# Performance work log

Measured on AMD Instinct MI355X. Metric: run time of the kernel, lower is better.

The kernel has to match this reference:

```python
import jax, jax.numpy as jnp
import numpy as np

EPS = 1e-6
B, N, I, H, O, L = 8, 2048, 64, 128, 8, 3
K = O * L
ITERS, TAU, LAM, KNN = 3, 0.1, 0.5, 5

def _ln(x, g, b):
    m = x.mean(-1, keepdims=True)
    v = jnp.mean((x - m) ** 2, -1, keepdims=True)
    return (x - m) / jnp.sqrt(v + 1e-5) * g + b

def _gelu(x):
    return jax.nn.gelu(x, approximate=False)


def setup_inputs():
    ks = jax.random.split(jax.random.key(0), 16)
    rn = lambda k, sh, s=0.05: jax.random.normal(k, sh, jnp.float32) * s
    return {
        'x': jax.random.normal(ks[0], (B, N, I), jnp.float32),
        'enc_w1': rn(ks[1], (H, I)), 'enc_b1': jnp.zeros((H,), jnp.float32),
        'enc_g1': jnp.ones((H,), jnp.float32), 'enc_bb1': jnp.zeros((H,), jnp.float32),
        'enc_w2': rn(ks[2], (H, H)), 'enc_b2': jnp.zeros((H,), jnp.float32),
        'enc_g2': jnp.ones((H,), jnp.float32), 'enc_bb2': jnp.zeros((H,), jnp.float32),
        'sp_w1': rn(ks[3], (H, H + 1)), 'sp_b1': jnp.zeros((H,), jnp.float32),
        'sp_g': jnp.ones((H,), jnp.float32), 'sp_bb': jnp.zeros((H,), jnp.float32),
        'sp_w2': rn(ks[4], (1, H), 0.005), 'sp_b2': jnp.zeros((1,), jnp.float32),
        'object_space': rn(ks[5], (1, O, H), 0.1),
        'horizon_scale': jnp.float32(0.3),
        'level_times': jnp.array([1.0, 2.5, 4.0], jnp.float32),
        'base_horizons': jnp.array([0.9, 0.6, 0.3], jnp.float32),
        'gru_w_ih': rn(ks[6], (3 * H, H)), 'gru_w_hh': rn(ks[7], (3 * H, H)),
        'gru_b_ih': jnp.zeros((3 * H,), jnp.float32), 'gru_b_hh': jnp.zeros((3 * H,), jnp.float32),
        'mlp_w1': rn(ks[8], (H, H)), 'mlp_b1': jnp.zeros((H,), jnp.float32),
        'mlp_w2': rn(ks[9], (H, H)), 'mlp_b2': jnp.zeros((H,), jnp.float32),
        'norm_g': jnp.ones((H,), jnp.float32), 'norm_b': jnp.zeros((H,), jnp.float32),
    }


def reference(x, enc_w1, enc_b1, enc_g1, enc_bb1, enc_w2, enc_b2, enc_g2, enc_bb2, sp_w1, sp_b1, sp_g, sp_bb, sp_w2, sp_b2, object_space, horizon_scale, level_times, base_horizons, gru_w_ih, gru_w_hh, gru_b_ih, gru_b_hh, mlp_w1, mlp_b1, mlp_w2, mlp_b2, norm_g, norm_b):
    # feature encoder: Linear -> LN -> GELU -> Linear -> LN
    h = _gelu(_ln(x @ enc_w1.T + enc_b1, enc_g1, enc_bb1))
    spatial = _ln(h @ enc_w2.T + enc_b2, enc_g2, enc_bb2)  # (B,N,H)
    # local density via kNN mean distance (torch.cdist equivalent)
    sq = jnp.sum(x * x, -1)
    d2 = sq[:, :, None] + sq[:, None, :] - 2.0 * jnp.einsum('bnd,bmd->bnm', x, x)
    dist = jnp.sqrt(jnp.maximum(d2, 0.0))
    knn = -jax.lax.top_k(-dist, KNN + 1)[0]           # k+1 smallest, ascending
    density = jnp.tanh(knn[..., 1:].mean(-1))          # (B,N)
    # scale predictor: Linear -> LN -> GELU -> Linear -> Softplus
    s = jnp.concatenate([spatial, density[..., None]], -1)
    s = _gelu(_ln(s @ sp_w1.T + sp_b1, sp_g, sp_bb))
    pred_scale = jax.nn.softplus(s @ sp_w2.T + sp_b2)  # (B,N,1)
    pred_time = 5.0 - 1.5 * density[..., None] + 0.5 * pred_scale
    features = jnp.concatenate([pred_time, spatial], -1)  # (B,N,H+1)
    # scale-adaptive horizons, tiled object-major to match slot layout
    hz = jnp.clip(base_horizons[None, :, None] + (horizon_scale * (density - 0.5))[:, None, :], 0.1, 1.0)
    horizons = jnp.tile(hz, (1, O, 1))                 # (B,K,N)
    # worldlines
    obj = jnp.broadcast_to(object_space, (B, O, H))
    times = jnp.broadcast_to(jnp.tile(level_times, O)[None, :, None], (B, K, 1))
    slots = jnp.concatenate([times, jnp.repeat(obj, L, axis=1)], -1)  # (B,K,H+1)
    feats_sp = features[..., 1:]
    old_flat = obj.reshape(-1, H)
    attn = None
    for _ in range(ITERS):
        diff = features[:, None, :, :] - slots[:, :, None, :]  # (B,K,N,H+1)
        dt = diff[..., 0]
        dr2 = jnp.sum(diff[..., 1:] ** 2, -1)
        ls = dt * dt - dr2
        d_L = jnp.sign(ls) * jnp.sqrt(jnp.abs(ls) + EPS)
        r = jnp.sqrt(dr2)
        cone = horizons - r / (jnp.abs(dt) + EPS) - 10.0 * jax.nn.relu(-dt) - 5.0 * jax.nn.relu(r - jnp.abs(dt))
        logits = -jnp.abs(d_L) + LAM * jnp.tanh(cone)
        attn = jax.nn.softmax(logits / TAU, axis=1)      # softmax over slots
        w = attn / (attn.sum(2, keepdims=True) + 1e-8)
        upd = jnp.einsum('bkn,bnh->bkh', w, feats_sp)
        obj_upd = upd.reshape(B, O, L, H).sum(2).reshape(-1, H)
        # GRUCell (torch semantics)
        gi = obj_upd @ gru_w_ih.T + gru_b_ih
        gh = old_flat @ gru_w_hh.T + gru_b_hh
        gi_r, gi_z, gi_n = jnp.split(gi, 3, -1)
        gh_r, gh_z, gh_n = jnp.split(gh, 3, -1)
        rg = jax.nn.sigmoid(gi_r + gh_r)
        zg = jax.nn.sigmoid(gi_z + gh_z)
        ng = jnp.tanh(gi_n + rg * gh_n)
        new = ((1.0 - zg) * ng + zg * old_flat).reshape(B, O, H)
        t = _gelu(_ln(new, norm_g, norm_b) @ mlp_w1.T + mlp_b1) @ mlp_w2.T + mlp_b2
        new = new + 0.2 * t
        slots = jnp.concatenate([times, jnp.repeat(new, L, axis=1)], -1)
    return slots, attn, pred_time[..., 0], density
```

## Files before the change

### kernel.cpp

```cpp
#include <hip/hip_runtime.h>
#include <math.h>

constexpr int cB = 8, cN = 2048, cI = 64, cH = 128, cO = 8, cK = 24;
constexpr int ROWS = cB * cN;

constexpr size_t WS_SPATIAL = 0;
constexpr size_t WS_SQ      = WS_SPATIAL + (size_t)ROWS * cH;
constexpr size_t WS_GHS     = WS_SQ + ROWS;
constexpr size_t WS_NSQ0    = WS_GHS + (size_t)cO * 3 * cH;
constexpr size_t WS_NEWOBJ  = WS_NSQ0 + cO;
constexpr size_t WS_NSQ     = WS_NEWOBJ + (size_t)cB * cO * cH;
constexpr size_t WS_WFRAG   = WS_NSQ + (size_t)cB * cO;
constexpr size_t WS_UPD3    = WS_WFRAG + 45056;
constexpr size_t WS_S3      = WS_UPD3 + (size_t)3 * cB * cK * cH;
constexpr size_t WS_XBF     = WS_S3 + (size_t)3 * cB * cK;

constexpr size_t WF_W1H = 0;
constexpr size_t WF_W1L = 8192;
constexpr size_t WF_W2H = 16384;
constexpr size_t WF_W2L = 32768;
constexpr size_t WF_WHH = 49152;
constexpr size_t WF_WHL = 69632;

constexpr size_t OUT_SLOTS = 0;
constexpr size_t OUT_ATTN  = (size_t)cB * cK * 129;
constexpr size_t OUT_PT    = OUT_ATTN + (size_t)cB * cK * cN;
constexpr size_t OUT_DEN   = OUT_PT + (size_t)cB * cN;

typedef __attribute__((ext_vector_type(8))) short bf16x8;
typedef __attribute__((ext_vector_type(4))) float f32x4;

__device__ __forceinline__ float gelu_f(float v){
  return 0.5f * v * (1.f + erff(v * 0.70710678118654752440f));
}
__device__ __forceinline__ short f2bf(float f){
  unsigned u = __float_as_uint(f);
  u += 0x7fffu + ((u >> 16) & 1u);
  return (short)(u >> 16);
}
__device__ __forceinline__ float bf2f(short h){
  return __uint_as_float(((unsigned)(unsigned short)h) << 16);
}
__device__ __forceinline__ bf16x8 pack8(float4 a, float4 b){
  bf16x8 r;
  r[0]=f2bf(a.x); r[1]=f2bf(a.y); r[2]=f2bf(a.z); r[3]=f2bf(a.w);
  r[4]=f2bf(b.x); r[5]=f2bf(b.y); r[6]=f2bf(b.z); r[7]=f2bf(b.w);
  return r;
}
__device__ __forceinline__ float qred16(float a){
  a += __shfl_xor(a, 1); a += __shfl_xor(a, 2); a += __shfl_xor(a, 4); a += __shfl_xor(a, 8);
  return a;
}
#define INS6(T0,T1,T2,T3,T4,T5,X) { \
  float _o0=T0,_o1=T1,_o2=T2,_o3=T3,_o4=T4,_o5=T5; \
  T0 = fminf(_o0, X); \
  T1 = __builtin_amdgcn_fmed3f(_o0,_o1,X); \
  T2 = __builtin_amdgcn_fmed3f(_o1,_o2,X); \
  T3 = __builtin_amdgcn_fmed3f(_o2,_o3,X); \
  T4 = __builtin_amdgcn_fmed3f(_o3,_o4,X); \
  T5 = __builtin_amdgcn_fmed3f(_o4,_o5,X); \
}
__device__ __forceinline__ void load_split_frag(const float* buf, int off, bf16x8& hi, bf16x8& lo){
  float4 u0 = *(const float4*)&buf[off];
  float4 u1 = *(const float4*)&buf[off + 4];
  float v[8] = {u0.x,u0.y,u0.z,u0.w,u1.x,u1.y,u1.z,u1.w};
  #pragma unroll
  for (int i = 0; i < 8; ++i){
    short h = f2bf(v[i]);
    hi[i] = h;
    lo[i] = f2bf(v[i] - bf2f(h));
  }
}
__device__ __forceinline__ int lidx(int row, int col, int stride){
  return row * stride + (col ^ ((row & 3) << 3));
}

__global__ __launch_bounds__(256) void k_cvt_sq(const float* __restrict__ x, short* __restrict__ xbf,
                                                float* __restrict__ sq){
  int t = threadIdx.x;
  size_t base = (size_t)blockIdx.x * 2048;
  int r = t >> 3, e0 = (t & 7) * 8;
  const float4* xp = (const float4*)(x + base + (size_t)r * cI + e0);
  float4 v0 = xp[0], v1 = xp[1];
  *(bf16x8*)(xbf + base + (size_t)r * cI + e0) = pack8(v0, v1);
  float s = v0.x*v0.x + v0.y*v0.y + v0.z*v0.z + v0.w*v0.w
          + v1.x*v1.x + v1.y*v1.y + v1.z*v1.z + v1.w*v1.w;
  s += __shfl_xor(s, 1); s += __shfl_xor(s, 2); s += __shfl_xor(s, 4);
  if ((t & 7) == 0) sq[blockIdx.x * 32 + r] = s;
}

__global__ __launch_bounds__(256) void k_prep(const float* __restrict__ objsp, const float* __restrict__ w_hh,
                                              const float* __restrict__ b_hh,
                                              const float* __restrict__ ew1, const float* __restrict__ ew2,
                                              const float* __restrict__ spw1,
                                              float* __restrict__ ghs, float* __restrict__ nsq0,
                                              short* __restrict__ wf){
  int id = blockIdx.x * 256 + threadIdx.x;
  if (id < cO * 3 * cH){
    int o = id / (3 * cH), j = id % (3 * cH);
    const float* wr = w_hh + (size_t)j * cH;
    const float* ob = objsp + (size_t)o * cH;
    float a0=0,a1=0,a2=0,a3=0;
    #pragma unroll
    for (int h = 0; h < cH; h += 4){
      a0 += wr[h]*ob[h]; a1 += wr[h+1]*ob[h+1]; a2 += wr[h+2]*ob[h+2]; a3 += wr[h+3]*ob[h+3];
    }
    ghs[id] = (a0+a1)+(a2+a3) + b_hh[j];
  } else if (id < cO * 3 * cH + cO){
    int o = id - cO * 3 * cH;
    const float* ob = objsp + (size_t)o * cH;
    float s = 0.f;
    for (int h = 0; h < cH; ++h) s += ob[h]*ob[h];
    nsq0[o] = s;
  } else {
    int idx = id - (cO * 3 * cH + cO);
    if (idx >= 45056) return;
    float w; size_t hoff, loff;
    int e, nc;
    if (idx < 8192){
      e = idx; nc = 2;
      int i = e & 7, l = (e >> 3) & 63, r = e >> 9;
      int c = r % nc, ft = r / nc;
      int f = ft * 16 + (l & 15), k = c * 32 + (l >> 4) * 8 + i;
      w = ew1[f * cI + k];
      hoff = WF_W1H + e; loff = WF_W1L + e;
    } else if (idx < 24576){
      e = idx - 8192; nc = 4;
      int i = e & 7, l = (e >> 3) & 63, r = e >> 9;
      int c = r % nc, ft = r / nc;
      int f = ft * 16 + (l & 15), k = c * 32 + (l >> 4) * 8 + i;
      w = ew2[f * cH + k];
      hoff = WF_W2H + e; loff = WF_W2L + e;
    } else {
      e = idx - 24576; nc = 5;
      int i = e & 7, l = (e >> 3) & 63, r = e >> 9;
      int c = r % nc, ft = r / nc;
      int f = ft * 16 + (l & 15), k = c * 32 + (l >> 4) * 8 + i;
      w = (k < 129) ? spw1[f * 129 + k] : 0.f;
      hoff = WF_WHH + e; loff = WF_WHL + e;
    }
    short h = f2bf(w);
    wf[hoff] = h;
    wf[loff] = f2bf(w - bf2f(h));
  }
}

__global__ __launch_bounds__(256) void k_pairwise(const short* __restrict__ xbf, const float* __restrict__ sq,
                                                  float* __restrict__ den_out){
  __shared__ float cand[4][16][101];
  int b  = blockIdx.x >> 7;
  int rt = blockIdx.x & 127;
  int r0 = rt * 16;
  int lane = threadIdx.x & 63, w = threadIdx.x >> 6;
  const short* xb = xbf + (size_t)b * cN * cI;

  int arow = r0 + (lane & 15);
  int koff = (lane >> 4) * 8;
  const bf16x8* ap = (const bf16x8*)(xb + (size_t)arow * cI + koff);
  bf16x8 a0 = ap[0];
  bf16x8 a1 = ap[4];

  float sqr[4];
  int rg0 = r0 + ((lane >> 4) << 2);
  #pragma unroll
  for (int j = 0; j < 4; ++j) sqr[j] = sq[b * cN + rg0 + j];

  float t6[4][6];
  #pragma unroll
  for (int j = 0; j < 4; ++j){
    #pragma unroll
    for (int q = 0; q < 6; ++q) t6[j][q] = 3e38f;
  }

  int cbase = w * 512;
  #pragma unroll 2
  for (int ct = 0; ct < 32; ++ct){
    int col0 = cbase + ct * 16;
    int brow = col0 + (lane & 15);
    const bf16x8* bp = (const bf16x8*)(xb + (size_t)brow * cI + koff);
    bf16x8 b0 = bp[0];
    bf16x8 b1 = bp[4];
    f32x4 acc = {0.f, 0.f, 0.f, 0.f};
    acc = __builtin_amdgcn_mfma_f32_16x16x32_bf16(a0, b0, acc, 0, 0, 0);
    acc = __builtin_amdgcn_mfma_f32_16x16x32_bf16(a1, b1, acc, 0, 0, 0);
    float sqc = sq[b * cN + col0 + (lane & 15)];
    #pragma unroll
    for (int j = 0; j < 4; ++j){
      float d2 = sqr[j] + sqc - 2.f * acc[j];
      d2 = fmaxf(d2, 0.f);
      INS6(t6[j][0], t6[j][1], t6[j][2], t6[j][3], t6[j][4], t6[j][5], d2);
    }
  }
  int rloc = (lane >> 4) << 2;
  #pragma unroll
  for (int j = 0; j < 4; ++j){
    #pragma unroll
    for (int q = 0; q < 6; ++q) cand[w][rloc + j][(lane & 15) * 6 + q] = t6[j][q];
  }
  __syncthreads();
  int tt = threadIdx.x;
  if (tt < 64){
    int ww = tt >> 4, rr = tt & 15;
    const float* c = cand[ww][rr];
    float m0=3e38f,m1=3e38f,m2=3e38f,m3=3e38f,m4=3e38f,m5=3e38f;
    #pragma unroll
    for (int q = 0; q < 96; ++q){
      float v = c[q];
      INS6(m0, m1, m2, m3, m4, m5, v);
    }
    float* cw = cand[ww][rr];
    cw[0]=m0; cw[1]=m1; cw[2]=m2; cw[3]=m3; cw[4]=m4; cw[5]=m5;
  }
  __syncthreads();
  if (tt < 16){
    float m0=3e38f,m1=3e38f,m2=3e38f,m3=3e38f,m4=3e38f,m5=3e38f;
    #pragma unroll
    for (int ww = 0; ww < 4; ++ww){
      const float* c = cand[ww][tt];
      #pragma unroll
      for (int q = 0; q < 6; ++q){
        float v = c[q];
        INS6(m0, m1, m2, m3, m4, m5, v);
      }
    }
    float md = (sqrtf(m1)+sqrtf(m2)+sqrtf(m3)+sqrtf(m4)+sqrtf(m5)) * 0.2f;
    den_out[b * cN + r0 + tt] = tanhf(md);
  }
}

__global__ __launch_bounds__(128) void k_enc_head(const float* __restrict__ x, const float* __restrict__ den_in,
    const short* __restrict__ wf,
    const float* __restrict__ b1, const float* __restrict__ g1, const float* __restrict__ bb1,
    const float* __restrict__ b2, const float* __restrict__ g2, const float* __restrict__ bb2,
    const float* __restrict__ hb1, const float* __restrict__ hg, const float* __restrict__ hbb,
    const float* __restrict__ hw2, const float* __restrict__ hb2,
    float* __restrict__ spatial, float* __restrict__ pt_out){
  __shared__ __align__(16) float xs_[2][16 * 68];
  __shared__ __align__(16) float hs_[2][16 * 164];
  const int t = threadIdx.x, lane = t & 63, wv = t >> 6;
  const int row0 = blockIdx.x * 32 + wv * 16;
  float* xbuf = xs_[wv];
  float* hbuf = hs_[wv];
  const int r15 = lane & 15, q = lane >> 4;
  const int qx = (q ^ (r15 & 3)) << 3;

  {
    const float4* xg = (const float4*)(x + (size_t)row0 * cI);
    #pragma unroll
    for (int k = 0; k < 4; ++k){
      int f4 = k * 64 + lane;
      int row = f4 >> 4, c4 = (f4 & 15) * 4;
      float4 v = xg[f4];
      *(float4*)&xbuf[lidx(row, c4, 68)] = v;
    }
  }
  __syncthreads();

  f32x4 acc[8];
  const short* w1h = wf + WF_W1H; const short* w1l = wf + WF_W1L;
  const short* w2h = wf + WF_W2H; const short* w2l = wf + WF_W2L;
  const short* whh = wf + WF_WHH; const short* whl = wf + WF_WHL;

  #pragma unroll
  for (int ft = 0; ft < 8; ++ft) acc[ft] = (f32x4){0.f,0.f,0.f,0.f};
  #pragma unroll
  for (int c = 0; c < 2; ++c){
    bf16x8 ah, al;
    load_split_frag(xbuf, r15 * 68 + c * 32 + qx, ah, al);
    #pragma unroll
    for (int ft = 0; ft < 8; ++ft){
      bf16x8 bh = *(const bf16x8*)&w1h[(size_t)(((ft*2 + c)*64) + lane) * 8];
      bf16x8 bl = *(const bf16x8*)&w1l[(size_t)(((ft*2 + c)*64) + lane) * 8];
      acc[ft] = __builtin_amdgcn_mfma_f32_16x16x32_bf16(al, bh, acc[ft], 0, 0, 0);
      acc[ft] = __builtin_amdgcn_mfma_f32_16x16x32_bf16(ah, bl, acc[ft], 0, 0, 0);
      acc[ft] = __builtin_amdgcn_mfma_f32_16x16x32_bf16(ah, bh, acc[ft], 0, 0, 0);
    }
  }
  {
    float sm0=0,sm1=0,sm2=0,sm3=0, s20=0,s21=0,s22=0,s23=0;
    #pragma unroll
    for (int ft = 0; ft < 8; ++ft){
      float bv = b1[ft*16 + r15];
      float v0 = acc[ft][0]+bv, v1 = acc[ft][1]+bv, v2 = acc[ft][2]+bv, v3 = acc[ft][3]+bv;
      acc[ft][0]=v0; acc[ft][1]=v1; acc[ft][2]=v2; acc[ft][3]=v3;
      sm0+=v0; sm1+=v1; sm2+=v2; sm3+=v3;
      s20+=v0*v0; s21+=v1*v1; s22+=v2*v2; s23+=v3*v3;
    }
    sm0=qred16(sm0); sm1=qred16(sm1); sm2=qred16(sm2); sm3=qred16(sm3);
    s20=qred16(s20); s21=qred16(s21); s22=qred16(s22); s23=qred16(s23);
    float mean[4] = { sm0*(1.f/128.f), sm1*(1.f/128.f), sm2*(1.f/128.f), sm3*(1.f/128.f) };
    float rstd[4] = { rsqrtf(s20*(1.f/128.f)-mean[0]*mean[0]+1e-5f),
                      rsqrtf(s21*(1.f/128.f)-mean[1]*mean[1]+1e-5f),
                      rsqrtf(s22*(1.f/128.f)-mean[2]*mean[2]+1e-5f),
                      rsqrtf(s23*(1.f/128.f)-mean[3]*mean[3]+1e-5f) };
    #pragma unroll
    for (int ft = 0; ft < 8; ++ft){
      float gv = g1[ft*16 + r15], bbv = bb1[ft*16 + r15];
      #pragma unroll
      for (int j = 0; j < 4; ++j){
        float e = gelu_f((acc[ft][j]-mean[j])*rstd[j]*gv + bbv);
        hbuf[lidx(q*4 + j, ft*16 + r15, 164)] = e;
      }
    }
  }
  __syncthreads();

  #pragma unroll
  for (int ft = 0; ft < 8; ++ft) acc[ft] = (f32x4){0.f,0.f,0.f,0.f};
  #pragma unroll
  for (int c = 0; c < 4; ++c){
    bf16x8 ah, al;
    load_split_frag(hbuf, r15 * 164 + c * 32 + qx, ah, al);
    #pragma unroll
    for (int ft = 0; ft < 8; ++ft){
      bf16x8 bh = *(const bf16x8*)&w2h[(size_t)(((ft*4 + c)*64) + lane) * 8];
      bf16x8 bl = *(const bf16x8*)&w2l[(size_t)(((ft*4 + c)*64) + lane) * 8];
      acc[ft] = __builtin_amdgcn_mfma_f32_16x16x32_bf16(al, bh, acc[ft], 0, 0, 0);
      acc[ft] = __builtin_amdgcn_mfma_f32_16x16x32_bf16(ah, bl, acc[ft], 0, 0, 0);
      acc[ft] = __builtin_amdgcn_mfma_f32_16x16x32_bf16(ah, bh, acc[ft], 0, 0, 0);
    }
  }
  __syncthreads();
  {
    float sm0=0,sm1=0,sm2=0,sm3=0, s20=0,s21=0,s22=0,s23=0;
    #pragma unroll
    for (int ft = 0; ft < 8; ++ft){
      float bv = b2[ft*16 + r15];
      float v0 = acc[ft][0]+bv, v1 = acc[ft][1]+bv, v2 = acc[ft][2]+bv, v3 = acc[ft][3]+bv;
      acc[ft][0]=v0; acc[ft][1]=v1; acc[ft][2]=v2; acc[ft][3]=v3;
      sm0+=v0; sm1+=v1; sm2+=v2; sm3+=v3;
      s20+=v0*v0; s21+=v1*v1; s22+=v2*v2; s23+=v3*v3;
    }
    sm0=qred16(sm0); sm1=qred16(sm1); sm2=qred16(sm2); sm3=qred16(sm3);
    s20=qred16(s20); s21=qred16(s21); s22=qred16(s22); s23=qred16(s23);
    float mean[4] = { sm0*(1.f/128.f), sm1*(1.f/128.f), sm2*(1.f/128.f), sm3*(1.f/128.f) };
    float rstd[4] = { rsqrtf(s20*(1.f/128.f)-mean[0]*mean[0]+1e-5f),
                      rsqrtf(s21*(1.f/128.f)-mean[1]*mean[1]+1e-5f),
                      rsqrtf(s22*(1.f/128.f)-mean[2]*mean[2]+1e-5f),
                      rsqrtf(s23*(1.f/128.f)-mean[3]*mean[3]+1e-5f) };
    #pragma unroll
    for (int ft = 0; ft < 8; ++ft){
      float gv = g2[ft*16 + r15], bbv = bb2[ft*16 + r15];
      #pragma unroll
      for (int j = 0; j < 4; ++j){
        float s = (acc[ft][j]-mean[j])*rstd[j]*gv + bbv;
        hbuf[lidx(q*4 + j, ft*16 + r15, 164)] = s;
      }
    }
    #pragma unroll
    for (int i = 0; i < 8; ++i){
      int flat = lane * 8 + i;
      int row = flat >> 5, col = 128 + (flat & 31);
      float v = ((flat & 31) == 0) ? den_in[row0 + row] : 0.f;
      hbuf[lidx(row, col, 164)] = v;
    }
  }
  __syncthreads();

  {
    #pragma unroll
    for (int k = 0; k < 8; ++k){
      int f4 = k * 64 + lane;
      int row = f4 >> 5, c4 = (f4 & 31) * 4;
      float4 v = *(const float4*)&hbuf[lidx(row, c4, 164)];
      *(float4*)(spatial + (size_t)(row0 + row) * cH + c4) = v;
    }
  }

  #pragma unroll
  for (int ft = 0; ft < 8; ++ft) acc[ft] = (f32x4){0.f,0.f,0.f,0.f};
  #pragma unroll
  for (int c = 0; c < 5; ++c){
    bf16x8 ah, al;
    load_split_frag(hbuf, r15 * 164 + c * 32 + qx, ah, al);
    #pragma unroll
    for (int ft = 0; ft < 8; ++ft){
      bf16x8 bh = *(const bf16x8*)&whh[(size_t)(((ft*5 + c)*64) + lane) * 8];
      bf16x8 bl = *(const bf16x8*)&whl[(size_t)(((ft*5 + c)*64) + lane) * 8];
      acc[ft] = __builtin_amdgcn_mfma_f32_16x16x32_bf16(al, bh, acc[ft], 0, 0, 0);
      acc[ft] = __builtin_amdgcn_mfma_f32_16x16x32_bf16(ah, bl, acc[ft], 0, 0, 0);
      acc[ft] = __builtin_amdgcn_mfma_f32_16x16x32_bf16(ah, bh, acc[ft], 0, 0, 0);
    }
  }
  {
    float sm0=0,sm1=0,sm2=0,sm3=0, s20=0,s21=0,s22=0,s23=0;
    #pragma unroll
    for (int ft = 0; ft < 8; ++ft){
      float bv = hb1[ft*16 + r15];
      float v0 = acc[ft][0]+bv, v1 = acc[ft][1]+bv, v2 = acc[ft][2]+bv, v3 = acc[ft][3]+bv;
      acc[ft][0]=v0; acc[ft][1]=v1; acc[ft][2]=v2; acc[ft][3]=v3;
      sm0+=v0; sm1+=v1; sm2+=v2; sm3+=v3;
      s20+=v0*v0; s21+=v1*v1; s22+=v2*v2; s23+=v3*v3;
    }
    sm0=qred16(sm0); sm1=qred16(sm1); sm2=qred16(sm2); sm3=qred16(sm3);
    s20=qred16(s20); s21=qred16(s21); s22=qred16(s22); s23=qred16(s23);
    float mean[4] = { sm0*(1.f/128.f), sm1*(1.f/128.f), sm2*(1.f/128.f), sm3*(1.f/128.f) };
    float rstd[4] = { rsqrtf(s20*(1.f/128.f)-mean[0]*mean[0]+1e-5f),
                      rsqrtf(s21*(1.f/128.f)-mean[1]*mean[1]+1e-5f),
                      rsqrtf(s22*(1.f/128.f)-mean[2]*mean[2]+1e-5f),
                      rsqrtf(s23*(1.f/128.f)-mean[3]*mean[3]+1e-5f) };
    float part0=0, part1=0, part2=0, part3=0;
    #pragma unroll
    for (int ft = 0; ft < 8; ++ft){
      float gv = hg[ft*16 + r15], bbv = hbb[ft*16 + r15], w2v = hw2[ft*16 + r15];
      part0 += gelu_f((acc[ft][0]-mean[0])*rstd[0]*gv + bbv) * w2v;
      part1 += gelu_f((acc[ft][1]-mean[1])*rstd[1]*gv + bbv) * w2v;
      part2 += gelu_f((acc[ft][2]-mean[2])*rstd[2]*gv + bbv) * w2v;
      part3 += gelu_f((acc[ft][3]-mean[3])*rstd[3]*gv + bbv) * w2v;
    }
    part0=qred16(part0); part1=qred16(part1); part2=qred16(part2); part3=qred16(part3);
    float parts[4] = { part0, part1, part2, part3 };
    #pragma unroll
    for (int j = 0; j < 4; ++j){
      if (r15 == j){
        int row = q * 4 + j;
        float ps = parts[j] + hb2[0];
        float spl = fmaxf(ps, 0.f) + log1pf(expf(-fabsf(ps)));
        float dn = den_in[row0 + row];
        pt_out[row0 + row] = 5.f - 1.5f*dn + 0.5f*spl;
      }
    }
  }
}

__global__ __launch_bounds__(256) void k_attn_upd(const float* __restrict__ spatial, const float* __restrict__ pt_in,
    const float* __restrict__ den_in, const float* __restrict__ objp, int ob_stride,
    const float* __restrict__ nsqp, int nq_stride,
    const float* __restrict__ lt, const float* __restrict__ bh, const float* __restrict__ hs,
    float* __restrict__ attn_out, int writeAttn,
    float* __restrict__ upd_raw, float* __restrict__ Ssum){
  __shared__ float abuf[24][33];
  int blk = blockIdx.x;
  int b = blk >> 6, chunk = blk & 63;
  int n0 = chunk * 32;
  int t = threadIdx.x;
  int sub = t & 7, rl = t >> 3;
  int id = b * cN + n0 + rl;

  {
    float4 sv[4];
    const float4* sp4 = (const float4*)(spatial + (size_t)id * cH + sub * 16);
    #pragma unroll
    for (int i = 0; i < 4; ++i) sv[i] = sp4[i];
    float spn2 = 0.f;
    #pragma unroll
    for (int i = 0; i < 4; ++i) spn2 += sv[i].x*sv[i].x + sv[i].y*sv[i].y + sv[i].z*sv[i].z + sv[i].w*sv[i].w;

    const float* ob = objp + (size_t)b * ob_stride;
    float acc[8];
    #pragma unroll
    for (int o = 0; o < 8; ++o){
      const float4* orow = (const float4*)(ob + (size_t)o * cH + sub * 16);
      float a0=0,a1=0,a2=0,a3=0;
      #pragma unroll
      for (int i = 0; i < 4; ++i){ float4 w4 = orow[i];
        a0 += w4.x*sv[i].x; a1 += w4.y*sv[i].y; a2 += w4.z*sv[i].z; a3 += w4.w*sv[i].w; }
      acc[o] = (a0+a1)+(a2+a3);
    }
    spn2 += __shfl_xor(spn2, 1); spn2 += __shfl_xor(spn2, 2); spn2 += __shfl_xor(spn2, 4);
    #pragma unroll
    for (int o = 0; o < 8; ++o){
      acc[o] += __shfl_xor(acc[o], 1); acc[o] += __shfl_xor(acc[o], 2); acc[o] += __shfl_xor(acc[o], 4);
    }

    if (sub == 0){
      const float* nq = nsqp + (size_t)b * nq_stride;
      float nsqv_[8];
      #pragma unroll
      for (int o = 0; o < 8; ++o) nsqv_[o] = nq[o];
      float pt = pt_in[id], den = den_in[id];
      float hsv = hs[0];
      float lts[3] = { lt[0], lt[1], lt[2] };
      float bhs[3] = { bh[0], bh[1], bh[2] };

      float logits[24];
      #pragma unroll
      for (int k = 0; k < 24; ++k){
        const int o = k / 3, l = k % 3;
        float dtv = pt - lts[l];
        float dr2 = fmaxf(spn2 + nsqv_[o] - 2.f * acc[o], 0.f);
        float ls  = dtv*dtv - dr2;
        float adL = sqrtf(fabsf(ls) + 1e-6f);
        float r   = sqrtf(dr2);
        float adt = fabsf(dtv);
        float hz  = fminf(fmaxf(bhs[l] + hsv * (den - 0.5f), 0.1f), 1.0f);
        float cone = hz - r / (adt + 1e-6f) - 10.f * fmaxf(-dtv, 0.f) - 5.f * fmaxf(r - adt, 0.f);
        logits[k] = (-adL + 0.5f * tanhf(cone)) * 10.f;
      }
      float mx = -3e38f;
      #pragma unroll
      for (int k = 0; k < 24; ++k) mx = fmaxf(mx, logits[k]);
      float es[24]; float ssum = 0.f;
      #pragma unroll
      for (int k = 0; k < 24; ++k){ es[k] = expf(logits[k] - mx); ssum += es[k]; }
      float inv = 1.f / ssum;
      #pragma unroll
      for (int k = 0; k < 24; ++k) abuf[k][rl] = es[k] * inv;
    }
  }
  __syncthreads();

  if (writeAttn){
    float* ao = attn_out + (size_t)b * cK * cN + n0;
    #pragma unroll
    for (int i = 0; i < 3; ++i){
      int idx = t + i * 256;
      ao[(size_t)(idx >> 5) * cN + (idx & 31)] = abuf[idx >> 5][idx & 31];
    }
  }

  int h = t & 127, g = t >> 7;
  float acc2[12];
  #pragma unroll
  for (int kk = 0; kk < 12; ++kk) acc2[kk] = 0.f;
  const float* sp = spatial + ((size_t)b * cN + n0) * cH + h;
  for (int ni = 0; ni < 32; ++ni){
    float spv = sp[(size_t)ni * cH];
    #pragma unroll
    for (int kk = 0; kk < 12; ++kk) acc2[kk] += abuf[g*12+kk][ni] * spv;
  }
  #pragma unroll
  for (int kk = 0; kk < 12; ++kk)
    atomicAdd(&upd_raw[((size_t)b * cK + g*12+kk) * cH + h], acc2[kk]);
  if (t < 24){
    float s = 0.f;
    #pragma unroll
    for (int j = 0; j < 32; ++j) s += abuf[t][j];
    atomicAdd(&Ssum[b * cK + t], s);
  }
}

__global__ __launch_bounds__(128) void k_gru(const float* __restrict__ upd_raw, const float* __restrict__ Ssum,
    const float* __restrict__ ghs, const float* __restrict__ objsp,
    const float* __restrict__ w_ih, const float* __restrict__ b_ih,
    const float* __restrict__ mw1, const float* __restrict__ mb1,
    const float* __restrict__ mw2, const float* __restrict__ mb2,
    const float* __restrict__ ng_, const float* __restrict__ nb_,
    const float* __restrict__ lt,
    float* __restrict__ newobj, float* __restrict__ nsq,
    float* __restrict__ slots_out, int writeSlots){
  __shared__ float ubuf[cH], lbuf[cH], gbuf[cH], red[8];
  int bo = blockIdx.x; int b = bo >> 3, o = bo & 7;
  int t = threadIdx.x;
  int lane = t & 63, wid = t >> 6;

  float u = 0.f;
  #pragma unroll
  for (int l = 0; l < 3; ++l){
    int k = o * 3 + l;
    float s = Ssum[b * cK + k] + 1e-8f;
    u += upd_raw[((size_t)b * cK + k) * cH + t] / s;
  }
  ubuf[t] = u;
  __syncthreads();

  float gi[3];
  #pragma unroll
  for (int j3 = 0; j3 < 3; ++j3){
    const float* wr = w_ih + ((size_t)j3 * cH + t) * cH;
    float a0=0,a1=0,a2=0,a3=0;
    #pragma unroll
    for (int d = 0; d < cH; d += 4){
      a0 += wr[d]*ubuf[d]; a1 += wr[d+1]*ubuf[d+1]; a2 += wr[d+2]*ubuf[d+2]; a3 += wr[d+3]*ubuf[d+3];
    }
    gi[j3] = (a0+a1)+(a2+a3) + b_ih[j3 * cH + t];
  }
  const float* gh = ghs + (size_t)o * 3 * cH;
  float ghr = gh[t], ghz = gh[cH + t], ghn = gh[2 * cH + t];
  float oldv = objsp[(size_t)o * cH + t];
  float rg = 1.f / (1.f + expf(-(gi[0] + ghr)));
  float zg = 1.f / (1.f + expf(-(gi[1] + ghz)));
  float ngv = tanhf(gi[2] + rg * ghn);
  float nv = (1.f - zg) * ngv + zg * oldv;

  float s1 = nv, s2 = nv * nv;
  #pragma unroll
  for (int m = 1; m < 64; m <<= 1){ s1 += __shfl_xor(s1, m); s2 += __shfl_xor(s2, m); }
  if (lane == 0){ red[wid] = s1; red[4 + wid] = s2; }
  __syncthreads();
  float mean = (red[0] + red[1]) * (1.f/128.f);
  float var  = (red[4] + red[5]) * (1.f/128.f) - mean * mean;
  float ln = (nv - mean) * rsqrtf(var + 1e-5f) * ng_[t] + nb_[t];
  lbuf[t] = ln;
  __syncthreads();

  const float* w1r = mw1 + (size_t)t * cH;
  {
    float a0=0,a1=0,a2=0,a3=0;
    #pragma unroll
    for (int d = 0; d < cH; d += 4){
      a0 += w1r[d]*lbuf[d]; a1 += w1r[d+1]*lbuf[d+1]; a2 += w1r[d+2]*lbuf[d+2]; a3 += w1r[d+3]*lbuf[d+3];
    }
    gbuf[t] = gelu_f((a0+a1)+(a2+a3) + mb1[t]);
  }
  __syncthreads();
  const float* w2r = mw2 + (size_t)t * cH;
  float m2v;
  {
    float a0=0,a1=0,a2=0,a3=0;
    #pragma unroll
    for (int d = 0; d < cH; d += 4){
      a0 += w2r[d]*gbuf[d]; a1 += w2r[d+1]*gbuf[d+1]; a2 += w2r[d+2]*gbuf[d+2]; a3 += w2r[d+3]*gbuf[d+3];
    }
    m2v = (a0+a1)+(a2+a3) + mb2[t];
  }
  float outv = nv + 0.2f * m2v;
  newobj[((size_t)b * cO + o) * cH + t] = outv;

  float qv = outv * outv;
  #pragma unroll
  for (int m = 1; m < 64; m <<= 1) qv += __shfl_xor(qv, m);
  __syncthreads();
  if (lane == 0) red[wid] = qv;
  __syncthreads();
  if (t == 0) nsq[b * cO + o] = red[0] + red[1];

  if (writeSlots){
    #pragma unroll
    for (int l = 0; l < 3; ++l){
      size_t base = ((size_t)b * cK + o * 3 + l) * 129;
      slots_out[base + 1 + t] = outv;
      if (t == 0) slots_out[base] = lt[l];
    }
  }
}

extern "C" void kernel_launch(void* const* d_in, const int* in_sizes, int n_in,
                              void* d_out, int out_size, void* d_ws, size_t ws_size,
                              hipStream_t stream){
  const float* x       = (const float*)d_in[0];
  const float* enc_w1  = (const float*)d_in[1];
  const float* enc_b1  = (const float*)d_in[2];
  const float* enc_g1  = (const float*)d_in[3];
  const float* enc_bb1 = (const float*)d_in[4];
  const float* enc_w2  = (const float*)d_in[5];
  const float* enc_b2  = (const float*)d_in[6];
  const float* enc_g2  = (const float*)d_in[7];
  const float* enc_bb2 = (const float*)d_in[8];
  const float* sp_w1   = (const float*)d_in[9];
  const float* sp_b1   = (const float*)d_in[10];
  const float* sp_g    = (const float*)d_in[11];
  const float* sp_bb   = (const float*)d_in[12];
  const float* sp_w2   = (const float*)d_in[13];
  const float* sp_b2   = (const float*)d_in[14];
  const float* objsp   = (const float*)d_in[15];
  const float* hscale  = (const float*)d_in[16];
  const float* ltimes  = (const float*)d_in[17];
  const float* bhor    = (const float*)d_in[18];
  const float* gw_ih   = (const float*)d_in[19];
  const float* gw_hh   = (const float*)d_in[20];
  const float* gb_ih   = (const float*)d_in[21];
  const float* gb_hh   = (const float*)d_in[22];
  const float* mw1     = (const float*)d_in[23];
  const float* mb1     = (const float*)d_in[24];
  const float* mw2     = (const float*)d_in[25];
  const float* mb2     = (const float*)d_in[26];
  const float* normg   = (const float*)d_in[27];
  const float* normb   = (const float*)d_in[28];
  (void)in_sizes; (void)n_in; (void)out_size; (void)ws_size;

  float* out = (float*)d_out;
  float* ws  = (float*)d_ws;

  float* spatial = ws + WS_SPATIAL;
  float* sq      = ws + WS_SQ;
  float* ghs     = ws + WS_GHS;
  float* nsq0    = ws + WS_NSQ0;
  float* newobj  = ws + WS_NEWOBJ;
  float* nsqv    = ws + WS_NSQ;
  short* wf      = (short*)(ws + WS_WFRAG);
  float* updr3   = ws + WS_UPD3;
  float* Ss3     = ws + WS_S3;
  short* xbf     = (short*)(ws + WS_XBF);

  hipMemsetAsync((void*)updr3, 0, (size_t)(3 * cB * cK * cH + 3 * cB * cK) * sizeof(float), stream);

  k_cvt_sq<<<dim3(ROWS / 32), dim3(256), 0, stream>>>(x, xbf, sq);
  k_prep<<<dim3(189), dim3(256), 0, stream>>>(objsp, gw_hh, gb_hh, enc_w1, enc_w2, sp_w1,
                                              ghs, nsq0, wf);
  k_pairwise<<<dim3(cB * (cN / 16)), dim3(256), 0, stream>>>(xbf, sq, out + OUT_DEN);
  k_enc_head<<<dim3(ROWS / 32), dim3(128), 0, stream>>>(x, out + OUT_DEN, wf,
      enc_b1, enc_g1, enc_bb1, enc_b2, enc_g2, enc_bb2,
      sp_b1, sp_g, sp_bb, sp_w2, sp_b2,
      spatial, out + OUT_PT);

  for (int it = 0; it < 3; ++it){
    float* updr = updr3 + (size_t)it * cB * cK * cH;
    float* Ss   = Ss3 + (size_t)it * cB * cK;
    const float* objp = (it == 0) ? objsp : newobj;
    int obst = (it == 0) ? 0 : cO * cH;
    const float* nqp = (it == 0) ? nsq0 : nsqv;
    int nqst = (it == 0) ? 0 : cO;
    k_attn_upd<<<dim3(cB * 64), dim3(256), 0, stream>>>(spatial, out + OUT_PT, out + OUT_DEN,
                                                        objp, obst, nqp, nqst,
                                                        ltimes, bhor, hscale,
                                                        out + OUT_ATTN, (it == 2) ? 1 : 0,
                                                        updr, Ss);
    k_gru<<<dim3(cB * cO), dim3(128), 0, stream>>>(updr, Ss, ghs, objsp, gw_ih, gb_ih,
                                                   mw1, mb1, mw2, mb2, normg, normb, ltimes,
                                                   newobj, nsqv, out + OUT_SLOTS, (it == 2) ? 1 : 0);
  }
}
```

Measured before the change: 303.3 us.

## Merge setup kernels and memset into one launch; skip top-k inserts early

Folds the bf16 conversion and squared-norm kernel, the weight-prep kernel and the workspace memset into a single k_setup kernel, assigning each job its own block range. This removes two launches and a memset from the stream. The kNN top-6 insertion in k_pairwise and its reduction now runs only when the candidate beats the current sixth-best. That branch saves median-network work but can cause wave divergence in the hot loop.

```diff
diff --git a/kernel.cpp b/kernel.cpp
--- a/kernel.cpp
+++ b/kernel.cpp
@@ -22,6 +22,9 @@
 constexpr size_t WF_WHH = 49152;
 constexpr size_t WF_WHL = 69632;
 
+constexpr int ZERO_FLOATS = 3 * cB * cK * cH + 3 * cB * cK;
+constexpr int ZERO_F4     = ZERO_FLOATS / 4;
+
 constexpr size_t OUT_SLOTS = 0;
 constexpr size_t OUT_ATTN  = (size_t)cB * cK * 129;
 constexpr size_t OUT_PT    = OUT_ATTN + (size_t)cB * cK * cN;
@@ -75,73 +78,82 @@
   return row * stride + (col ^ ((row & 3) << 3));
 }
 
-__global__ __launch_bounds__(256) void k_cvt_sq(const float* __restrict__ x, short* __restrict__ xbf,
-                                                float* __restrict__ sq){
+__global__ __launch_bounds__(256) void k_setup(const float* __restrict__ x, short* __restrict__ xbf,
+                                               float* __restrict__ sq,
+                                               const float* __restrict__ objsp, const float* __restrict__ w_hh,
+                                               const float* __restrict__ b_hh,
+                                               const float* __restrict__ ew1, const float* __restrict__ ew2,
+                                               const float* __restrict__ spw1,
+                                               float* __restrict__ ghs, float* __restrict__ nsq0,
+                                               short* __restrict__ wf,
+                                               float* __restrict__ zero_base){
+  int bid = blockIdx.x;
   int t = threadIdx.x;
-  size_t base = (size_t)blockIdx.x * 2048;
-  int r = t >> 3, e0 = (t & 7) * 8;
-  const float4* xp = (const float4*)(x + base + (size_t)r * cI + e0);
-  float4 v0 = xp[0], v1 = xp[1];
-  *(bf16x8*)(xbf + base + (size_t)r * cI + e0) = pack8(v0, v1);
-  float s = v0.x*v0.x + v0.y*v0.y + v0.z*v0.z + v0.w*v0.w
-          + v1.x*v1.x + v1.y*v1.y + v1.z*v1.z + v1.w*v1.w;
-  s += __shfl_xor(s, 1); s += __shfl_xor(s, 2); s += __shfl_xor(s, 4);
-  if ((t & 7) == 0) sq[blockIdx.x * 32 + r] = s;
-}
-
-__global__ __launch_bounds__(256) void k_prep(const float* __restrict__ objsp, const float* __restrict__ w_hh,
-                                              const float* __restrict__ b_hh,
-                                              const float* __restrict__ ew1, const float* __restrict__ ew2,
-                                              const float* __restrict__ spw1,
-                                              float* __restrict__ ghs, float* __restrict__ nsq0,
-                                              short* __restrict__ wf){
-  int id = blockIdx.x * 256 + threadIdx.x;
-  if (id < cO * 3 * cH){
-    int o = id / (3 * cH), j = id % (3 * cH);
-    const float* wr = w_hh + (size_t)j * cH;
-    const float* ob = objsp + (size_t)o * cH;
-    float a0=0,a1=0,a2=0,a3=0;
-    #pragma unroll
-    for (int h = 0; h < cH; h += 4){
-      a0 += wr[h]*ob[h]; a1 += wr[h+1]*ob[h+1]; a2 += wr[h+2]*ob[h+2]; a3 += wr[h+3]*ob[h+3];
-    }
-    ghs[id] = (a0+a1)+(a2+a3) + b_hh[j];
-  } else if (id < cO * 3 * cH + cO){
-    int o = id - cO * 3 * cH;
-    const float* ob = objsp + (size_t)o * cH;
-    float s = 0.f;
-    for (int h = 0; h < cH; ++h) s += ob[h]*ob[h];
-    nsq0[o] = s;
+  if (bid < 512){
+    size_t base = (size_t)bid * 2048;
+    int r = t >> 3, e0 = (t & 7) * 8;
+    const float4* xp = (const float4*)(x + base + (size_t)r * cI + e0);
+    float4 v0 = xp[0], v1 = xp[1];
+    *(bf16x8*)(xbf + base + (size_t)r * cI + e0) = pack8(v0, v1);
+    float s = v0.x*v0.x + v0.y*v0.y + v0.z*v0.z + v0.w*v0.w
+            + v1.x*v1.x + v1.y*v1.y + v1.z*v1.z + v1.w*v1.w;
+    s += __shfl_xor(s, 1); s += __shfl_xor(s, 2); s += __shfl_xor(s, 4);
+    if ((t & 7) == 0) sq[bid * 32 + r] = s;
+  } else if (bid < 701){
+    int id = (bid - 512) * 256 + t;
+    if (id < cO * 3 * cH){
+      int o = id / (3 * cH), j = id % (3 * cH);
+      const float* wr = w_hh + (size_t)j * cH;
+      const float* ob = objsp + (size_t)o * cH;
+      float a0=0,a1=0,a2=0,a3=0;
+      #pragma unroll
+      for (int h = 0; h < cH; h += 4){
+        a0 += wr[h]*ob[h]; a1 += wr[h+1]*ob[h+1]; a2 += wr[h+2]*ob[h+2]; a3 += wr[h+3]*ob[h+3];
+      }
+      ghs[id] = (a0+a1)+(a2+a3) + b_hh[j];
+    } else if (id < cO * 3 * cH + cO){
+      int o = id - cO * 3 * cH;
+      const float* ob = objsp + (size_t)o * cH;
+      float s = 0.f;
+      for (int h = 0; h < cH; ++h) s += ob[h]*ob[h];
+      nsq0[o] = s;
+    } else {
+      int idx = id - (cO * 3 * cH + cO);
+      if (idx >= 45056) return;
+      float w; size_t hoff, loff;
+      int e, nc;
+      if (idx < 8192){
+        e = idx; nc = 2;
+        int i = e & 7, l = (e >> 3) & 63, r = e >> 9;
+        int c = r % nc, ft = r / nc;
+        int f = ft * 16 + (l & 15), k = c * 32 + (l >> 4) * 8 + i;
+        w = ew1[f * cI + k];
+        hoff = WF_W1H + e; loff = WF_W1L + e;
+      } else if (idx < 24576){
+        e = idx - 8192; nc = 4;
+        int i = e & 7, l = (e >> 3) & 63, r = e >> 9;
+        int c = r % nc, ft = r / nc;
+        int f = ft * 16 + (l & 15), k = c * 32 + (l >> 4) * 8 + i;
+        w = ew2[f * cH + k];
+        hoff = WF_W2H + e; loff = WF_W2L + e;
+      } else {
+        e = idx - 24576; nc = 5;
+        int i = e & 7, l = (e >> 3) & 63, r = e >> 9;
+        int c = r % nc, ft = r / nc;
+        int f = ft * 16 + (l & 15), k = c * 32 + (l >> 4) * 8 + i;
+        w = (k < 129) ? spw1[f * 129 + k] : 0.f;
+        hoff = WF_WHH + e; loff = WF_WHL + e;
+      }
+      short h = f2bf(w);
+      wf[hoff] = h;
+      wf[loff] = f2bf(w - bf2f(h));
+    }
   } else {
-    int idx = id - (cO * 3 * cH + cO);
-    if (idx >= 45056) return;
-    float w; size_t hoff, loff;
-    int e, nc;
-    if (idx < 8192){
-      e = idx; nc = 2;
-      int i = e & 7, l = (e >> 3) & 63, r = e >> 9;
-      int c = r % nc, ft = r / nc;
-      int f = ft * 16 + (l & 15), k = c * 32 + (l >> 4) * 8 + i;
-      w = ew1[f * cI + k];
-      hoff = WF_W1H + e; loff = WF_W1L + e;
-    } else if (idx < 24576){
-      e = idx - 8192; nc = 4;
-      int i = e & 7, l = (e >> 3) & 63, r = e >> 9;
-      int c = r % nc, ft = r / nc;
-      int f = ft * 16 + (l & 15), k = c * 32 + (l >> 4) * 8 + i;
-      w = ew2[f * cH + k];
-      hoff = WF_W2H + e; loff = WF_W2L + e;
-    } else {
-      e = idx - 24576; nc = 5;
-      int i = e & 7, l = (e >> 3) & 63, r = e >> 9;
-      int c = r % nc, ft = r / nc;
-      int f = ft * 16 + (l & 15), k = c * 32 + (l >> 4) * 8 + i;
-      w = (k < 129) ? spw1[f * 129 + k] : 0.f;
-      hoff = WF_WHH + e; loff = WF_WHL + e;
-    }
-    short h = f2bf(w);
-    wf[hoff] = h;
-    wf[loff] = f2bf(w - bf2f(h));
+    int idx = (bid - 701) * 256 + t;
+    if (idx < ZERO_F4){
+      float4 z = {0.f, 0.f, 0.f, 0.f};
+      *(float4*)(zero_base + (size_t)idx * 4) = z;
+    }
   }
 }
 
@@ -188,7 +200,9 @@
     for (int j = 0; j < 4; ++j){
       float d2 = sqr[j] + sqc - 2.f * acc[j];
       d2 = fmaxf(d2, 0.f);
-      INS6(t6[j][0], t6[j][1], t6[j][2], t6[j][3], t6[j][4], t6[j][5], d2);
+      if (d2 < t6[j][5]){
+        INS6(t6[j][0], t6[j][1], t6[j][2], t6[j][3], t6[j][4], t6[j][5], d2);
+      }
     }
   }
   int rloc = (lane >> 4) << 2;
@@ -206,7 +220,9 @@
     #pragma unroll
     for (int q = 0; q < 96; ++q){
       float v = c[q];
-      INS6(m0, m1, m2, m3, m4, m5, v);
+      if (v < m5){
+        INS6(m0, m1, m2, m3, m4, m5, v);
+      }
     }
     float* cw = cand[ww][rr];
     cw[0]=m0; cw[1]=m1; cw[2]=m2; cw[3]=m3; cw[4]=m4; cw[5]=m5;
@@ -673,11 +689,9 @@
   float* Ss3     = ws + WS_S3;
   short* xbf     = (short*)(ws + WS_XBF);
 
-  hipMemsetAsync((void*)updr3, 0, (size_t)(3 * cB * cK * cH + 3 * cB * cK) * sizeof(float), stream);
-
-  k_cvt_sq<<<dim3(ROWS / 32), dim3(256), 0, stream>>>(x, xbf, sq);
-  k_prep<<<dim3(189), dim3(256), 0, stream>>>(objsp, gw_hh, gb_hh, enc_w1, enc_w2, sp_w1,
-                                              ghs, nsq0, wf);
+  k_setup<<<dim3(774), dim3(256), 0, stream>>>(x, xbf, sq,
+                                               objsp, gw_hh, gb_hh, enc_w1, enc_w2, sp_w1,
+                                               ghs, nsq0, wf, updr3);
   k_pairwise<<<dim3(cB * (cN / 16)), dim3(256), 0, stream>>>(xbf, sq, out + OUT_DEN);
   k_enc_head<<<dim3(ROWS / 32), dim3(128), 0, stream>>>(x, out + OUT_DEN, wf,
       enc_b1, enc_g1, enc_bb1, enc_b2, enc_g2, enc_bb2,
```

New measurement: 299.3 us. Within noise of the previous version (-1.3%).
